# Kernel tuning notes

Measured on AMD Instinct MI355X. Metric: run time of the kernel, lower is better.

Reference implementation:

```python
import jax, jax.numpy as jnp
import numpy as np

B, T, D, H = 4, 4096, 1024, 16
DH = D // H
NB = T // 2 + 1  # rfft bins


def setup_inputs() -> dict:
    key = jax.random.key(0)
    ks = jax.random.split(key, 6)
    x = jax.random.normal(ks[0], (B, T, D), dtype=jnp.float32)
    # torch nn.Linear params: weight [out, in], bias [out]
    W_qkv = jax.random.normal(ks[1], (3 * D, D), dtype=jnp.float32) * 0.02
    b_qkv = jnp.zeros((3 * D,), dtype=jnp.float32)
    W_o = jax.random.normal(ks[2], (D, D), dtype=jnp.float32) * 0.02
    b_o = jnp.zeros((D,), dtype=jnp.float32)
    # per-head per-bin spectral filters (smart-init-like small values)
    log_gain = jax.random.normal(ks[3], (H, NB), dtype=jnp.float32) * 0.05
    phase = jax.random.normal(ks[4], (H, NB), dtype=jnp.float32) * 0.01
    return {"x": x, "W_qkv": W_qkv, "b_qkv": b_qkv, "W_o": W_o,
            "b_o": b_o, "log_gain": log_gain, "phase": phase}


def reference(x, W_qkv, b_qkv, W_o, b_o, log_gain, phase):
    # qkv projection; only v is used on the spectral path (q,k discarded)
    qkv = jnp.einsum('btd,ed->bte', x, W_qkv) + b_qkv  # [B,T,3D]
    v = qkv[..., 2 * D:]                               # [B,T,D]
    v = v.reshape(B, T, H, DH).transpose(0, 2, 1, 3)   # [B,H,T,DH]
    # rFFT along the token dim
    v_f = jnp.fft.rfft(v.astype(jnp.float32), axis=2)  # [B,H,NB,DH] complex
    # per-head per-bin complex filter: polar(exp(log_gain), phase)
    mag = jnp.exp(log_gain)
    comp = jax.lax.complex(mag * jnp.cos(phase), mag * jnp.sin(phase))  # [H,NB]
    v_f = v_f * comp[None, :, :, None]
    y_h = jnp.fft.irfft(v_f, n=T, axis=2)              # [B,H,T,DH]
    y = y_h.transpose(0, 2, 1, 3).reshape(B, T, D)     # [B,T,D]
    y = jnp.einsum('btd,ed->bte', y, W_o) + b_o
    return x + y
```

## Files before the change

### kernel.cpp

```cpp
#include <hip/hip_runtime.h>
#include <hip/hip_bf16.h>
#include <math.h>

#define B_BATCH 4
#define T_LEN   4096
#define D_DIM   1024
#define H_HEADS 16
#define NB_BINS 2049
#define M_ROWS  (B_BATCH * T_LEN)

typedef __attribute__((ext_vector_type(8))) short short8;
typedef __attribute__((ext_vector_type(8))) unsigned short u16x8;
typedef __attribute__((ext_vector_type(4))) float f32x4;

__device__ __forceinline__ ushort f2bf(float f) {
    unsigned b = __float_as_uint(f);
    unsigned r = (b + 0x7fffu + ((b >> 16) & 1u)) >> 16;
    return (ushort)r;
}
__device__ __forceinline__ float bf2f(ushort u) {
    return __uint_as_float(((unsigned)u) << 16);
}

__global__ void cvt_f32_to_bf16(const float* __restrict__ src, ushort* __restrict__ dst, int n4) {
    int i = blockIdx.x * 256 + threadIdx.x;
    if (i >= n4) return;
    float4 v = ((const float4*)src)[i];
    ushort4 o;
    o.x = f2bf(v.x); o.y = f2bf(v.y); o.z = f2bf(v.z); o.w = f2bf(v.w);
    ((ushort4*)dst)[i] = o;
}

__global__ void cvt_weights(const float* __restrict__ wv, const float* __restrict__ wo,
                            ushort* __restrict__ wvb, ushort* __restrict__ wob, int n4) {
    int i = blockIdx.x * 256 + threadIdx.x;
    const float* src = (i < n4) ? wv : wo;
    ushort* dst = (i < n4) ? wvb : wob;
    int j = (i < n4) ? i : (i - n4);
    float4 v = ((const float4*)src)[j];
    ushort4 o;
    o.x = f2bf(v.x); o.y = f2bf(v.y); o.z = f2bf(v.z); o.w = f2bf(v.w);
    ((ushort4*)dst)[j] = o;
}

__device__ __forceinline__ int drev16(int i) {
    return ((i & 15) << 8) | (i & 0xF0) | (i >> 8);
}

__global__ void prep_tables(const float* __restrict__ lg, const float* __restrict__ ph,
                            float2* __restrict__ Cdr, float2* __restrict__ tw) {
    int idx = blockIdx.x * 256 + threadIdx.x;
    if (idx < 4096) {
        double th = -2.0 * 3.14159265358979323846 * (double)idx / 4096.0;
        tw[idx] = make_float2((float)cos(th), (float)sin(th));
    }
    if (idx >= H_HEADS * 4096) return;
    int h = idx >> 12, i = idx & 4095;
    int f = drev16(i);
    int fc = (f <= 2048) ? f : (4096 - f);
    float sgn = (f <= 2048) ? 1.f : -1.f;
    float m = expf(lg[h * NB_BINS + fc]) * (1.0f / 4096.0f);
    float p = ph[h * NB_BINS + fc];
    float re = m * __cosf(p), im = sgn * m * __sinf(p);
    if (fc == 0 || fc == 2048) im = 0.f;
    Cdr[idx] = make_float2(re, im);
}

template<bool RESID, bool BIASROW>
__global__ __launch_bounds__(512, 1) void gemm256(const ushort* __restrict__ A,
        const ushort* __restrict__ Bm, const float* __restrict__ bias,
        const float* __restrict__ resid, void* __restrict__ Cout,
        int M, int N, int K) {
    __shared__ ushort lds[65536];
    const int tid  = threadIdx.x;
    const int lane = tid & 63;
    const int wid  = tid >> 6;
    const int wr   = wid >> 2, wc = wid & 3;
    const int fr   = lane & 15;
    const int nbn  = N >> 8;
    int bid = (int)blockIdx.x;
    bid = (bid & 7) * ((int)gridDim.x >> 3) + (bid >> 3);
    const int bm = bid / nbn, bn = bid % nbn;
    const int row0 = bm << 8, col0 = bn << 8;
    const int NT = K >> 6;

    f32x4 acc[8][4];
#pragma unroll
    for (int i = 0; i < 8; i++)
#pragma unroll
        for (int j = 0; j < 4; j++) acc[i][j] = (f32x4){0.f, 0.f, 0.f, 0.f};

    auto stageA = [&](int t, int s) {
        int base = (((t & 1) << 1) + s) << 13;
        int k0 = (t << 6) + (s << 5);
#pragma unroll
        for (int i = 0; i < 2; i++) {
            int r = (wid << 5) + (i << 4) + (lane >> 2);
            int c = ((lane & 3) ^ ((lane >> 3) & 3)) << 3;
            const ushort* g = A + (size_t)(row0 + r) * (size_t)K + (size_t)(k0 + c);
            __builtin_amdgcn_global_load_lds(
                (const __attribute__((address_space(1))) void*)g,
                (__attribute__((address_space(3))) void*)&lds[base + (((wid << 1) + i) << 9)],
                16, 0, 0);
        }
    };
    auto stageB = [&](int t, int s) {
        int base = 32768 + ((((t & 1) << 1) + s) << 13);
        int k0 = (t << 6) + (s << 5);
#pragma unroll
        for (int i = 0; i < 2; i++) {
            int r = (wid << 5) + (i << 4) + (lane >> 2);
            int c = ((lane & 3) ^ ((lane >> 3) & 3)) << 3;
            const ushort* g = Bm + (size_t)(col0 + r) * (size_t)K + (size_t)(k0 + c);
            __builtin_amdgcn_global_load_lds(
                (const __attribute__((address_space(1))) void*)g,
                (__attribute__((address_space(3))) void*)&lds[base + (((wid << 1) + i) << 9)],
                16, 0, 0);
        }
    };
    auto rdfrag = [&](int base, int row) -> short8 {
        int g = (((lane >> 4) ^ ((row >> 1) & 3)) << 3);
        return *(const short8*)&lds[base + (row << 5) + g];
    };

    stageA(0, 0); stageA(0, 1); stageB(0, 0); stageB(0, 1);
    __syncthreads();

    for (int t = 0; t < NT; ++t) {
        const int d = t & 1;
        if (t + 1 < NT) {
            stageA(t + 1, 0); stageA(t + 1, 1);
            stageB(t + 1, 0); stageB(t + 1, 1);
        }
#pragma unroll
        for (int ks = 0; ks < 2; ks++) {
            const int ab = (((d << 1) + ks) << 13);
            const int bb = 32768 + (((d << 1) + ks) << 13);
            short8 bF[4], aF[4];
#pragma unroll
            for (int ni = 0; ni < 4; ni++) bF[ni] = rdfrag(bb, (wc << 6) + (ni << 4) + fr);
#pragma unroll
            for (int mh = 0; mh < 2; mh++) {
#pragma unroll
                for (int mi = 0; mi < 4; mi++)
                    aF[mi] = rdfrag(ab, (wr << 7) + (mh << 6) + (mi << 4) + fr);
#pragma unroll
                for (int mi = 0; mi < 4; mi++)
#pragma unroll
                    for (int ni = 0; ni < 4; ni++)
                        acc[(mh << 2) + mi][ni] = __builtin_amdgcn_mfma_f32_16x16x32_bf16(
                            aF[mi], bF[ni], acc[(mh << 2) + mi][ni], 0, 0, 0);
            }
        }
        __syncthreads();
    }

    const int crow = (lane >> 4) << 2;
#pragma unroll
    for (int mi = 0; mi < 8; mi++) {
#pragma unroll
        for (int ni = 0; ni < 4; ni++) {
            int row = row0 + (wr << 7) + (mi << 4) + crow;
            int col = col0 + (wc << 6) + (ni << 4) + fr;
            float bcol = BIASROW ? 0.f : bias[col];
#pragma unroll
            for (int j = 0; j < 4; j++) {
                float v = acc[mi][ni][j] + (BIASROW ? bias[row + j] : bcol);
                size_t off = (size_t)(row + j) * N + col;
                if (RESID) ((float*)Cout)[off] = resid[off] + v;
                else       ((ushort*)Cout)[off] = f2bf(v);
            }
        }
    }
}

__device__ __forceinline__ float2 cadd(float2 a, float2 b){ return make_float2(a.x+b.x, a.y+b.y); }
__device__ __forceinline__ float2 csub(float2 a, float2 b){ return make_float2(a.x-b.x, a.y-b.y); }
__device__ __forceinline__ float2 jmulp(float2 z){ return make_float2(-z.y, z.x); }
__device__ __forceinline__ float2 cmul(float2 a, float2 b){
    return make_float2(fmaf(a.x,b.x,-a.y*b.y), fmaf(a.x,b.y, a.y*b.x)); }
__device__ __forceinline__ float2 cmulc(float2 a, float2 b){
    return make_float2(fmaf(a.x,b.x, a.y*b.y), fmaf(a.y,b.x,-a.x*b.y)); }

template<int INV>
__device__ __forceinline__ void bf4(float2& a, float2& b, float2& c, float2& d) {
    float2 acp = cadd(a,c), acm = csub(a,c);
    float2 bdp = cadd(b,d), bdm = csub(b,d);
    float2 jb  = jmulp(bdm);
    a = cadd(acp, bdp);
    c = csub(acp, bdp);
    if (INV) { b = cadd(acm, jb); d = csub(acm, jb); }
    else     { b = csub(acm, jb); d = cadd(acm, jb); }
}

#define C16_1 0.9238795325112867f
#define S16_1 0.3826834323650898f
#define R16_2 0.7071067811865476f

template<int INV>
__device__ __forceinline__ void dft16(float2 v[16]) {
    const float sg = INV ? 1.f : -1.f;
    bf4<INV>(v[0], v[4], v[8],  v[12]);
    bf4<INV>(v[1], v[5], v[9],  v[13]);
    bf4<INV>(v[2], v[6], v[10], v[14]);
    bf4<INV>(v[3], v[7], v[11], v[15]);
    const float2 w1 = make_float2( C16_1, sg*S16_1);
    const float2 w2 = make_float2( R16_2, sg*R16_2);
    const float2 w3 = make_float2( S16_1, sg*C16_1);
    const float2 w6 = make_float2(-R16_2, sg*R16_2);
    const float2 w9 = make_float2(-C16_1,-sg*S16_1);
    v[5]  = cmul(v[5],  w1);
    v[6]  = cmul(v[6],  w2);
    v[7]  = cmul(v[7],  w3);
    v[9]  = cmul(v[9],  w2);
    v[10] = INV ? jmulp(v[10]) : make_float2(v[10].y, -v[10].x);
    v[11] = cmul(v[11], w6);
    v[13] = cmul(v[13], w3);
    v[14] = cmul(v[14], w6);
    v[15] = cmul(v[15], w9);
    bf4<INV>(v[0],  v[1],  v[2],  v[3]);
    bf4<INV>(v[4],  v[5],  v[6],  v[7]);
    bf4<INV>(v[8],  v[9],  v[10], v[11]);
    bf4<INV>(v[12], v[13], v[14], v[15]);
}

__host__ __device__ constexpr int oidx(int r) { return ((r & 3) << 2) | (r >> 2); }

template<int INV>
__device__ __forceinline__ void dft16p(float2 v[16]) {
    const float sg = INV ? 1.f : -1.f;
    bf4<INV>(v[oidx(0)], v[oidx(4)], v[oidx(8)],  v[oidx(12)]);
    bf4<INV>(v[oidx(1)], v[oidx(5)], v[oidx(9)],  v[oidx(13)]);
    bf4<INV>(v[oidx(2)], v[oidx(6)], v[oidx(10)], v[oidx(14)]);
    bf4<INV>(v[oidx(3)], v[oidx(7)], v[oidx(11)], v[oidx(15)]);
    const float2 w1 = make_float2( C16_1, sg*S16_1);
    const float2 w2 = make_float2( R16_2, sg*R16_2);
    const float2 w3 = make_float2( S16_1, sg*C16_1);
    const float2 w6 = make_float2(-R16_2, sg*R16_2);
    const float2 w9 = make_float2(-C16_1,-sg*S16_1);
    v[oidx(5)]  = cmul(v[oidx(5)],  w1);
    v[oidx(6)]  = cmul(v[oidx(6)],  w2);
    v[oidx(7)]  = cmul(v[oidx(7)],  w3);
    v[oidx(9)]  = cmul(v[oidx(9)],  w2);
    v[oidx(10)] = INV ? jmulp(v[oidx(10)]) : make_float2(v[oidx(10)].y, -v[oidx(10)].x);
    v[oidx(11)] = cmul(v[oidx(11)], w6);
    v[oidx(13)] = cmul(v[oidx(13)], w3);
    v[oidx(14)] = cmul(v[oidx(14)], w6);
    v[oidx(15)] = cmul(v[oidx(15)], w9);
    bf4<INV>(v[oidx(0)],  v[oidx(1)],  v[oidx(2)],  v[oidx(3)]);
    bf4<INV>(v[oidx(4)],  v[oidx(5)],  v[oidx(6)],  v[oidx(7)]);
    bf4<INV>(v[oidx(8)],  v[oidx(9)],  v[oidx(10)], v[oidx(11)]);
    bf4<INV>(v[oidx(12)], v[oidx(13)], v[oidx(14)], v[oidx(15)]);
}

__device__ __forceinline__ int phz(int t) { return t ^ (((t >> 4) ^ (t >> 8)) & 15); }

template<typename F>
__device__ __forceinline__ void tw_powers(float2 w1, F&& apply) {
    apply(1, w1);
    float2 w2 = cmul(w1, w1);   apply(2, w2);
    float2 w3 = cmul(w2, w1);   apply(3, w3);
    float2 w4 = cmul(w2, w2);   apply(4, w4);
    float2 w5 = cmul(w4, w1);   apply(5, w5);
    float2 w6 = cmul(w4, w2);   apply(6, w6);
    float2 w7 = cmul(w4, w3);   apply(7, w7);
    float2 w8 = cmul(w4, w4);   apply(8, w8);
    apply(9,  cmul(w8, w1));
    apply(10, cmul(w8, w2));
    apply(11, cmul(w8, w3));
    apply(12, cmul(w8, w4));
    apply(13, cmul(w8, w5));
    apply(14, cmul(w8, w6));
    apply(15, cmul(w8, w7));
}

__global__ __launch_bounds__(256) void fft16_filter(const ushort* __restrict__ VT,
                                                    ushort* __restrict__ yT,
                                                    const float2* __restrict__ tw,
                                                    const float2* __restrict__ Cdr) {
    __shared__ float2 X[2][4096];
    const int tid = threadIdx.x;
    const int b   = blockIdx.x >> 8;
    const int qb  = blockIdx.x & 255;
    const int d0  = qb << 2;
    const int h   = qb >> 4;

    float2 v[2][16];
#pragma unroll
    for (int p = 0; p < 2; p++) {
        const ushort* sRe = VT + (size_t)(d0 + 2 * p) * M_ROWS + b * T_LEN;
        const ushort* sIm = VT + (size_t)(d0 + 2 * p + 1) * M_ROWS + b * T_LEN;
#pragma unroll
        for (int j = 0; j < 16; j++)
            v[p][j] = make_float2(bf2f(sRe[tid + (j << 8)]), bf2f(sIm[tid + (j << 8)]));
    }

    dft16<0>(v[0]);
    dft16<0>(v[1]);
    {
        float2 w1 = tw[tid];
        tw_powers(w1, [&](int r, float2 w) {
            v[0][oidx(r)] = cmul(v[0][oidx(r)], w);
            v[1][oidx(r)] = cmul(v[1][oidx(r)], w);
        });
    }
#pragma unroll
    for (int r = 0; r < 16; r++) {
        int a = phz(tid + (r << 8));
        X[0][a] = v[0][oidx(r)];
        X[1][a] = v[1][oidx(r)];
    }
    __syncthreads();

    const int p2 = tid & 15, g2 = tid >> 4;
    const int base2 = (g2 << 8) + p2;
#pragma unroll
    for (int j = 0; j < 16; j++) {
        int a = phz(base2 + (j << 4));
        v[0][j] = X[0][a];
        v[1][j] = X[1][a];
    }
    dft16<0>(v[0]);
    dft16<0>(v[1]);
#pragma unroll
    for (int r = 1; r < 16; r++) {
        float2 w = tw[(p2 * r) << 4];
        v[0][oidx(r)] = cmul(v[0][oidx(r)], w);
        v[1][oidx(r)] = cmul(v[1][oidx(r)], w);
    }
#pragma unroll
    for (int r = 0; r < 16; r++) {
        int a = phz(base2 + (r << 4));
        X[0][a] = v[0][oidx(r)];
        X[1][a] = v[1][oidx(r)];
    }
    __syncthreads();

    const int base3 = tid << 4;
#pragma unroll
    for (int j = 0; j < 16; j++) {
        int a = phz(base3 + j);
        v[0][j] = X[0][a];
        v[1][j] = X[1][a];
    }
    dft16<0>(v[0]);
    dft16<0>(v[1]);
    const float2* Ch = Cdr + (h << 12) + base3;
#pragma unroll
    for (int r = 0; r < 16; r++) {
        float2 c = Ch[r];
        v[0][oidx(r)] = cmul(v[0][oidx(r)], c);
        v[1][oidx(r)] = cmul(v[1][oidx(r)], c);
    }
    dft16p<1>(v[0]);
    dft16p<1>(v[1]);
#pragma unroll
    for (int r = 0; r < 16; r++) {
        int a = phz(base3 + r);
        X[0][a] = v[0][r];
        X[1][a] = v[1][r];
    }
    __syncthreads();

#pragma unroll
    for (int j = 0; j < 16; j++) {
        int a = phz(base2 + (j << 4));
        v[0][j] = X[0][a];
        v[1][j] = X[1][a];
    }
#pragma unroll
    for (int j = 1; j < 16; j++) {
        float2 w = tw[(p2 * j) << 4];
        v[0][j] = cmulc(v[0][j], w);
        v[1][j] = cmulc(v[1][j], w);
    }
    dft16<1>(v[0]);
    dft16<1>(v[1]);
#pragma unroll
    for (int r = 0; r < 16; r++) {
        int a = phz(base2 + (r << 4));
        X[0][a] = v[0][oidx(r)];
        X[1][a] = v[1][oidx(r)];
    }
    __syncthreads();

#pragma unroll
    for (int j = 0; j < 16; j++) {
        int a = phz(tid + (j << 8));
        v[0][j] = X[0][a];
        v[1][j] = X[1][a];
    }
    {
        float2 w1 = tw[tid];
        tw_powers(w1, [&](int r, float2 w) {
            v[0][r] = cmulc(v[0][r], w);
            v[1][r] = cmulc(v[1][r], w);
        });
    }
    dft16<1>(v[0]);
    dft16<1>(v[1]);
#pragma unroll
    for (int p = 0; p < 2; p++) {
        ushort* dRe = yT + (size_t)(d0 + 2 * p) * M_ROWS + b * T_LEN;
        ushort* dIm = yT + (size_t)(d0 + 2 * p + 1) * M_ROWS + b * T_LEN;
#pragma unroll
        for (int r = 0; r < 16; r++) {
            float2 val = v[p][oidx(r)];
            dRe[tid + (r << 8)] = f2bf(val.x);
            dIm[tid + (r << 8)] = f2bf(val.y);
        }
    }
}

__global__ __launch_bounds__(256) void transpose_yT(const ushort* __restrict__ src,
                                                    ushort* __restrict__ dst) {
    __shared__ ushort tile[4096];
    const int tid = threadIdx.x;
    const int bm = blockIdx.x & 255;
    const int bd = blockIdx.x >> 8;
    const int m0 = bm << 6, d0 = bd << 6;
#pragma unroll
    for (int i = 0; i < 2; i++) {
        int vn = tid + (i << 8);
        int r  = vn >> 3;
        int c8 = (vn & 7) << 3;
        u16x8 val = *(const u16x8*)&src[(size_t)(d0 + r) * M_ROWS + m0 + c8];
#pragma unroll
        for (int q = 0; q < 8; q++)
            tile[(r << 6) | ((c8 + q) ^ r)] = (ushort)val[q];
    }
    __syncthreads();
    const int dc = tid & 63;
    const int wb = tid >> 6;
#pragma unroll
    for (int i = 0; i < 16; i++) {
        int mr = wb + (i << 2);
        dst[(size_t)(m0 + mr) * D_DIM + d0 + dc] = tile[(dc << 6) | (mr ^ dc)];
    }
}

extern "C" void kernel_launch(void* const* d_in, const int* in_sizes, int n_in,
                              void* d_out, int out_size, void* d_ws, size_t ws_size,
                              hipStream_t stream) {
    const float* x    = (const float*)d_in[0];
    const float* Wqkv = (const float*)d_in[1];
    const float* bqkv = (const float*)d_in[2];
    const float* Wo   = (const float*)d_in[3];
    const float* bo   = (const float*)d_in[4];
    const float* lg   = (const float*)d_in[5];
    const float* ph   = (const float*)d_in[6];

    char* ws = (char*)d_ws;
    ushort* xb  = (ushort*)ws;
    ushort* Wvb = (ushort*)(ws + 33554432);
    ushort* Wob = (ushort*)(ws + 35651584);
    float2* tw  = (float2*)(ws + 37748736);
    float2* Cdr = (float2*)(ws + 37781504);

    ushort* VT   = (ushort*)d_out;
    ushort* yT   = (ushort*)((char*)d_out + 33554432);
    ushort* ynat = xb;
    float*  out  = (float*)d_out;

    prep_tables<<<(H_HEADS * 4096) / 256, 256, 0, stream>>>(lg, ph, Cdr, tw);
    cvt_f32_to_bf16<<<(16777216 / 4) / 256, 256, 0, stream>>>(x, xb, 16777216 / 4);
    cvt_weights<<<2 * (1048576 / 4) / 256, 256, 0, stream>>>(
        Wqkv + 2048 * 1024, Wo, Wvb, Wob, 1048576 / 4);

    gemm256<false, true><<<(D_DIM / 256) * (M_ROWS / 256), 512, 0, stream>>>(
        Wvb, xb, bqkv + 2 * D_DIM, nullptr, (void*)VT, D_DIM, M_ROWS, D_DIM);

    fft16_filter<<<B_BATCH * (D_DIM / 4), 256, 0, stream>>>(VT, yT, tw, Cdr);

    transpose_yT<<<(M_ROWS / 64) * (D_DIM / 64), 256, 0, stream>>>(yT, ynat);

    gemm256<true, false><<<(M_ROWS / 256) * (D_DIM / 256), 512, 0, stream>>>(
        ynat, Wob, bo, x, (void*)out, M_ROWS, D_DIM, D_DIM);
}
```

Baseline: 163.1 us.

## Fuse fp32-to-bf16 conversion of x into the V projection GEMM loader

Drops the standalone pass that converts x to bf16. The first GEMM now loads fp32 x tiles into registers, converts them to bf16 and writes them to LDS, with the global loads staged across the two k-substeps so they overlap the MFMA work. This removes a full read of x (64MB fp32) and a 32MB bf16 write-plus-reread. In exchange the GEMM reads twice as many bytes for its B operand and uses register-staged loads instead of direct global-to-LDS copies, which adds register pressure and VALU work inside the main loop.

New measurement: 159.3 us, median of 2. 2.4% less time.

```diff
diff --git a/kernel.cpp b/kernel.cpp
--- a/kernel.cpp
+++ b/kernel.cpp
@@ -21,14 +21,11 @@
 __device__ __forceinline__ float bf2f(ushort u) {
     return __uint_as_float(((unsigned)u) << 16);
 }
-
-__global__ void cvt_f32_to_bf16(const float* __restrict__ src, ushort* __restrict__ dst, int n4) {
-    int i = blockIdx.x * 256 + threadIdx.x;
-    if (i >= n4) return;
-    float4 v = ((const float4*)src)[i];
-    ushort4 o;
-    o.x = f2bf(v.x); o.y = f2bf(v.y); o.z = f2bf(v.z); o.w = f2bf(v.w);
-    ((ushort4*)dst)[i] = o;
+__device__ __forceinline__ u16x8 pack8(const float4& a, const float4& b) {
+    u16x8 o;
+    o[0] = f2bf(a.x); o[1] = f2bf(a.y); o[2] = f2bf(a.z); o[3] = f2bf(a.w);
+    o[4] = f2bf(b.x); o[5] = f2bf(b.y); o[6] = f2bf(b.z); o[7] = f2bf(b.w);
+    return o;
 }
 
 __global__ void cvt_weights(const float* __restrict__ wv, const float* __restrict__ wo,
@@ -66,9 +63,9 @@
     Cdr[idx] = make_float2(re, im);
 }
 
-template<bool RESID, bool BIASROW>
+template<bool RESID, bool BIASROW, bool BF32>
 __global__ __launch_bounds__(512, 1) void gemm256(const ushort* __restrict__ A,
-        const ushort* __restrict__ Bm, const float* __restrict__ bias,
+        const void* __restrict__ Bv, const float* __restrict__ bias,
         const float* __restrict__ resid, void* __restrict__ Cout,
         int M, int N, int K) {
     __shared__ ushort lds[65536];
@@ -84,6 +81,9 @@
     const int row0 = bm << 8, col0 = bn << 8;
     const int NT = K >> 6;
 
+    const ushort* Bu = (const ushort*)Bv;
+    const float*  Bf = (const float*)Bv;
+
     f32x4 acc[8][4];
 #pragma unroll
     for (int i = 0; i < 8; i++)
@@ -111,11 +111,32 @@
         for (int i = 0; i < 2; i++) {
             int r = (wid << 5) + (i << 4) + (lane >> 2);
             int c = ((lane & 3) ^ ((lane >> 3) & 3)) << 3;
-            const ushort* g = Bm + (size_t)(col0 + r) * (size_t)K + (size_t)(k0 + c);
+            const ushort* g = Bu + (size_t)(col0 + r) * (size_t)K + (size_t)(k0 + c);
             __builtin_amdgcn_global_load_lds(
                 (const __attribute__((address_space(1))) void*)g,
                 (__attribute__((address_space(3))) void*)&lds[base + (((wid << 1) + i) << 9)],
                 16, 0, 0);
+        }
+    };
+    auto issueB = [&](int t, int s, float4 bR[2][2]) {
+#pragma unroll
+        for (int i = 0; i < 2; i++) {
+            int row = (wid << 5) + (i << 4) + (lane >> 2);
+            int cc  = lane & 3;
+            const float* g = Bf + (size_t)(col0 + row) * (size_t)K
+                           + (size_t)((t << 6) + (s << 5) + (cc << 3));
+            bR[i][0] = *(const float4*)g;
+            bR[i][1] = *(const float4*)(g + 4);
+        }
+    };
+    auto writeB = [&](int t, int s, float4 bR[2][2]) {
+        int base = 32768 + ((((t & 1) << 1) + s) << 13);
+#pragma unroll
+        for (int i = 0; i < 2; i++) {
+            int row = (wid << 5) + (i << 4) + (lane >> 2);
+            int cc  = lane & 3;
+            int slot = cc ^ ((row >> 1) & 3);
+            *(u16x8*)&lds[base + (row << 5) + (slot << 3)] = pack8(bR[i][0], bR[i][1]);
         }
     };
     auto rdfrag = [&](int base, int row) -> short8 {
@@ -123,22 +144,31 @@
         return *(const short8*)&lds[base + (row << 5) + g];
     };
 
-    stageA(0, 0); stageA(0, 1); stageB(0, 0); stageB(0, 1);
+    stageA(0, 0); stageA(0, 1);
+    if (BF32) {
+        float4 bR0[2][2], bR1[2][2];
+        issueB(0, 0, bR0); issueB(0, 1, bR1);
+        writeB(0, 0, bR0); writeB(0, 1, bR1);
+    } else {
+        stageB(0, 0); stageB(0, 1);
+    }
     __syncthreads();
 
     for (int t = 0; t < NT; ++t) {
         const int d = t & 1;
-        if (t + 1 < NT) {
+        const bool pre = (t + 1) < NT;
+        float4 bR[2][2];
+        if (pre) {
             stageA(t + 1, 0); stageA(t + 1, 1);
-            stageB(t + 1, 0); stageB(t + 1, 1);
-        }
-#pragma unroll
-        for (int ks = 0; ks < 2; ks++) {
-            const int ab = (((d << 1) + ks) << 13);
-            const int bb = 32768 + (((d << 1) + ks) << 13);
-            short8 bF[4], aF[4];
-#pragma unroll
-            for (int ni = 0; ni < 4; ni++) bF[ni] = rdfrag(bb, (wc << 6) + (ni << 4) + fr);
+            if (BF32) issueB(t + 1, 0, bR);
+            else { stageB(t + 1, 0); stageB(t + 1, 1); }
+        }
+        {
+            const int ab = (((d << 1) + 0) << 13);
+            const int bb = 32768 + (((d << 1) + 0) << 13);
+            short8 bFr[4], aF[4];
+#pragma unroll
+            for (int ni = 0; ni < 4; ni++) bFr[ni] = rdfrag(bb, (wc << 6) + (ni << 4) + fr);
 #pragma unroll
             for (int mh = 0; mh < 2; mh++) {
 #pragma unroll
@@ -149,9 +179,30 @@
 #pragma unroll
                     for (int ni = 0; ni < 4; ni++)
                         acc[(mh << 2) + mi][ni] = __builtin_amdgcn_mfma_f32_16x16x32_bf16(
-                            aF[mi], bF[ni], acc[(mh << 2) + mi][ni], 0, 0, 0);
+                            aF[mi], bFr[ni], acc[(mh << 2) + mi][ni], 0, 0, 0);
             }
         }
+        if (BF32 && pre) { writeB(t + 1, 0, bR); issueB(t + 1, 1, bR); }
+        {
+            const int ab = (((d << 1) + 1) << 13);
+            const int bb = 32768 + (((d << 1) + 1) << 13);
+            short8 bFr[4], aF[4];
+#pragma unroll
+            for (int ni = 0; ni < 4; ni++) bFr[ni] = rdfrag(bb, (wc << 6) + (ni << 4) + fr);
+#pragma unroll
+            for (int mh = 0; mh < 2; mh++) {
+#pragma unroll
+                for (int mi = 0; mi < 4; mi++)
+                    aF[mi] = rdfrag(ab, (wr << 7) + (mh << 6) + (mi << 4) + fr);
+#pragma unroll
+                for (int mi = 0; mi < 4; mi++)
+#pragma unroll
+                    for (int ni = 0; ni < 4; ni++)
+                        acc[(mh << 2) + mi][ni] = __builtin_amdgcn_mfma_f32_16x16x32_bf16(
+                            aF[mi], bFr[ni], acc[(mh << 2) + mi][ni], 0, 0, 0);
+            }
+        }
+        if (BF32 && pre) writeB(t + 1, 1, bR);
         __syncthreads();
     }
 
@@ -451,7 +502,7 @@
     const float* ph   = (const float*)d_in[6];
 
     char* ws = (char*)d_ws;
-    ushort* xb  = (ushort*)ws;
+    ushort* ynat = (ushort*)ws;
     ushort* Wvb = (ushort*)(ws + 33554432);
     ushort* Wob = (ushort*)(ws + 35651584);
     float2* tw  = (float2*)(ws + 37748736);
@@ -459,21 +510,19 @@
 
     ushort* VT   = (ushort*)d_out;
     ushort* yT   = (ushort*)((char*)d_out + 33554432);
-    ushort* ynat = xb;
     float*  out  = (float*)d_out;
 
     prep_tables<<<(H_HEADS * 4096) / 256, 256, 0, stream>>>(lg, ph, Cdr, tw);
-    cvt_f32_to_bf16<<<(16777216 / 4) / 256, 256, 0, stream>>>(x, xb, 16777216 / 4);
     cvt_weights<<<2 * (1048576 / 4) / 256, 256, 0, stream>>>(
         Wqkv + 2048 * 1024, Wo, Wvb, Wob, 1048576 / 4);
 
-    gemm256<false, true><<<(D_DIM / 256) * (M_ROWS / 256), 512, 0, stream>>>(
-        Wvb, xb, bqkv + 2 * D_DIM, nullptr, (void*)VT, D_DIM, M_ROWS, D_DIM);
+    gemm256<false, true, true><<<(D_DIM / 256) * (M_ROWS / 256), 512, 0, stream>>>(
+        Wvb, (const void*)x, bqkv + 2 * D_DIM, nullptr, (void*)VT, D_DIM, M_ROWS, D_DIM);
 
     fft16_filter<<<B_BATCH * (D_DIM / 4), 256, 0, stream>>>(VT, yT, tw, Cdr);
 
     transpose_yT<<<(M_ROWS / 64) * (D_DIM / 64), 256, 0, stream>>>(yT, ynat);
 
-    gemm256<true, false><<<(M_ROWS / 256) * (D_DIM / 256), 512, 0, stream>>>(
-        ynat, Wob, bo, x, (void*)out, M_ROWS, D_DIM, D_DIM);
-}
+    gemm256<true, false, false><<<(M_ROWS / 256) * (D_DIM / 256), 512, 0, stream>>>(
+        ynat, (const void*)Wob, bo, x, (void*)out, M_ROWS, D_DIM, D_DIM);
+}
```
